# Kernel tuning notes

Measured on AMD Instinct MI355X. Metric: run time of the kernel, lower is better.

The kernel has to match this reference:

```python
import jax, jax.numpy as jnp
import numpy as np

N = 50000          # num nodes
E_RAND = 600000    # random edges (self-loops appended -> E = E_RAND + N)
HEADS = 4
OUT_CH = 16
OUT_NEURONS = 2 * OUT_CH   # diag reparam: [mean | std-logit]
IN_CH = 128
NEG_SLOPE = 0.2


def setup_inputs() -> dict:
    key = jax.random.key(0)
    k1, k2, k3, k4, k5 = jax.random.split(key, 5)
    x = jax.random.normal(k1, (N, IN_CH), jnp.float32)
    src = jax.random.randint(k2, (E_RAND,), 0, N, jnp.int32)
    dst = jax.random.randint(k3, (E_RAND,), 0, N, jnp.int32)
    loops = jnp.arange(N, dtype=jnp.int32)
    edge_index = jnp.stack([jnp.concatenate([src, loops]),
                            jnp.concatenate([dst, loops])])  # [2, E]
    # glorot init for weight [IN_CH, HEADS*OUT_NEURONS]
    s_w = float(np.sqrt(6.0 / (IN_CH + HEADS * OUT_NEURONS)))
    weight = jax.random.uniform(k4, (IN_CH, HEADS * OUT_NEURONS), jnp.float32, -s_w, s_w)
    # glorot for att [1, HEADS, 2*OUT_NEURONS]
    s_a = float(np.sqrt(6.0 / (HEADS + 2 * OUT_NEURONS)))
    att = jax.random.uniform(k5, (1, HEADS, 2 * OUT_NEURONS), jnp.float32, -s_a, s_a)
    bias = jnp.zeros((HEADS * OUT_NEURONS,), jnp.float32)
    return {"x": x, "edge_index": edge_index, "weight": weight, "att": att, "bias": bias}


def reference(x, edge_index, weight, att, bias):
    src, dst = edge_index[0], edge_index[1]  # j -> i (PyG source_to_target)
    h = (x @ weight).reshape(N, HEADS, OUT_NEURONS)          # Theta x
    x_j = h[src]                                             # [E, H, On]
    x_i = h[dst]                                             # [E, H, On]
    # alpha = LeakyReLU(a^T [x_i || x_j])
    alpha = (x_i * att[:, :, :OUT_NEURONS]).sum(-1) + \
            (x_j * att[:, :, OUT_NEURONS:]).sum(-1)          # [E, H]
    alpha = jax.nn.leaky_relu(alpha, NEG_SLOPE)
    # segment softmax over neighborhoods of target node i
    m = jax.ops.segment_max(alpha, dst, num_segments=N)      # [N, H]
    e = jnp.exp(alpha - m[dst])
    denom = jax.ops.segment_sum(e, dst, num_segments=N)      # [N, H]
    alpha = e / (denom[dst] + 1e-16)                          # [E, H]
    # scatter-add aggregation of attention-weighted features
    agg = jax.ops.segment_sum(x_j * alpha[:, :, None], dst, num_segments=N)  # [N, H, On]
    out = agg.reshape(N, HEADS * OUT_NEURONS) + bias
    # VIB diag reparameterization + closed-form KL against N(0, I)
    o = out.reshape(N * HEADS, OUT_NEURONS)
    mean = o[:, :OUT_CH]
    std = jax.nn.softplus(o[:, OUT_CH:] - 5.0) + 1e-10
    kl = (-jnp.log(std) + 0.5 * (std * std + mean * mean) - 0.5).sum(-1)  # [N*H]
    ixz = kl.reshape(N, HEADS).mean(-1)                      # [N]
    # eval + val_use_mean=True: output is the mean part
    out_final = mean.reshape(N, HEADS * OUT_CH)
    structure_kl_loss = jnp.zeros((), jnp.float32)
    return out_final, ixz, structure_kl_loss, mean, std
```

## Files before the change

kernel.cpp:

```cpp
#include <hip/hip_runtime.h>
#include <stdint.h>

#define NN 50000
#define NB 196
#define NEG_SLOPE 0.2f
#define WTS 136

#define IXZ_OFF    (NN * 64)
#define SKL_OFF    (NN * 64 + NN)
#define MEAN_OFF   (NN * 64 + NN + 1)
#define STD_OFF    (MEAN_OFF + NN * 64)

typedef unsigned int u32;
typedef unsigned short u16;
typedef __attribute__((ext_vector_type(8))) short short8;
typedef __attribute__((ext_vector_type(4))) float f32x4;

__device__ __forceinline__ float bf2f(u16 s) { return __uint_as_float(((u32)s) << 16); }
__device__ __forceinline__ u16 f2bf(float f) {
    u32 u = __float_as_uint(f);
    u += 0x7FFFu + ((u >> 16) & 1u);
    return (u16)(u >> 16);
}
__device__ __forceinline__ float lo16(u32 u) { return __uint_as_float(u << 16); }
__device__ __forceinline__ float hi16(u32 u) { return __uint_as_float(u & 0xFFFF0000u); }
__device__ __forceinline__ float red32(float v) {
    v += __shfl_xor(v, 16); v += __shfl_xor(v, 8); v += __shfl_xor(v, 4);
    v += __shfl_xor(v, 2);  v += __shfl_xor(v, 1);
    return v;
}
__device__ __forceinline__ float softplusf(float x) {
    return fmaxf(x, 0.f) + log1pf(expf(-fabsf(x)));
}
__device__ __forceinline__ void stout(void* o, long long idx, float v, bool f32) {
    if (f32) ((float*)o)[idx] = v;
    else     ((u16*)o)[idx]   = f2bf(v);
}
__device__ __forceinline__ int wscan_incl(int v, int lane) {
#pragma unroll
    for (int off = 1; off < 64; off <<= 1) {
        int u = __shfl_up(v, off);
        if (lane >= off) v += u;
    }
    return v;
}

__global__ void k_detect(const u32* __restrict__ xw, int* __restrict__ flag)
{
    int t = threadIdx.x;
    u32 wrd = xw[t];
    u32 e = (wrd >> 7) & 0xFF;
    bool plaus = (e >= 0x60 && e <= 0x85);
    unsigned long long b = __ballot(plaus);
    if (t == 0) flag[0] = (__popcll(b) < 32) ? 1 : 0;
}

__global__ __launch_bounds__(256) void k_wt(const void* __restrict__ wv_,
                                            const int* __restrict__ flag,
                                            u16* __restrict__ wtg)
{
    const int t = threadIdx.x;
    const int k = blockIdx.x * 16 + (t >> 4);
    const int cq = t & 15;
    const bool f32 = flag[0] != 0;
    u16 v[8];
    if (f32) {
        const float* w = (const float*)wv_;
        float4 a = *(const float4*)(w + k * 128 + cq * 8);
        float4 b = *(const float4*)(w + k * 128 + cq * 8 + 4);
        v[0] = f2bf(a.x); v[1] = f2bf(a.y); v[2] = f2bf(a.z); v[3] = f2bf(a.w);
        v[4] = f2bf(b.x); v[5] = f2bf(b.y); v[6] = f2bf(b.z); v[7] = f2bf(b.w);
    } else {
        const u16* w = (const u16*)wv_;
        uint4 u = *(const uint4*)(w + k * 128 + cq * 8);
        v[0] = (u16)(u.x & 0xFFFF); v[1] = (u16)(u.x >> 16);
        v[2] = (u16)(u.y & 0xFFFF); v[3] = (u16)(u.y >> 16);
        v[4] = (u16)(u.z & 0xFFFF); v[5] = (u16)(u.z >> 16);
        v[6] = (u16)(u.w & 0xFFFF); v[7] = (u16)(u.w >> 16);
    }
#pragma unroll
    for (int j = 0; j < 8; j++)
        wtg[(cq * 8 + j) * WTS + k] = v[j];
}

__global__ __launch_bounds__(256) void k_gemm(
    const void* __restrict__ xv, const u16* __restrict__ wtg,
    const void* __restrict__ attv, const int* __restrict__ flag,
    u16* __restrict__ hb, float* __restrict__ ai, float* __restrict__ aj)
{
    __shared__ __align__(16) u16 ls[128 * WTS];
    const int tid = threadIdx.x;
    const bool f32 = flag[0] != 0;

    {
        uint4* d = (uint4*)ls;
        const uint4* s = (const uint4*)wtg;
        for (int i = tid; i < 128 * WTS / 8; i += 256) d[i] = s[i];
    }

    const int w = tid >> 6, L = tid & 63;
    const int q = L >> 4, c15 = L & 15;
    const int nb16 = blockIdx.x * 64 + w * 16;

    short8 afr[4];
    {
        int nrow = nb16 + c15; if (nrow > NN - 1) nrow = NN - 1;
        if (f32) {
            const float* xp = (const float*)xv + (size_t)nrow * 128 + q * 8;
#pragma unroll
            for (int ks = 0; ks < 4; ks++) {
                float4 a = *(const float4*)(xp + ks * 32);
                float4 b = *(const float4*)(xp + ks * 32 + 4);
                union { short8 s; u16 e[8]; } u;
                u.e[0] = f2bf(a.x); u.e[1] = f2bf(a.y); u.e[2] = f2bf(a.z); u.e[3] = f2bf(a.w);
                u.e[4] = f2bf(b.x); u.e[5] = f2bf(b.y); u.e[6] = f2bf(b.z); u.e[7] = f2bf(b.w);
                afr[ks] = u.s;
            }
        } else {
            const u16* xp = (const u16*)xv + (size_t)nrow * 128 + q * 8;
#pragma unroll
            for (int ks = 0; ks < 4; ks++)
                afr[ks] = *(const short8*)(xp + ks * 32);
        }
    }
    __syncthreads();

    f32x4 acc[8];
#pragma unroll
    for (int t = 0; t < 8; t++) {
        acc[t] = (f32x4){0.f, 0.f, 0.f, 0.f};
        const u16* bp = ls + (16 * t + c15) * WTS + q * 8;
#pragma unroll
        for (int ks = 0; ks < 4; ks++) {
            short8 bfr = *(const short8*)(bp + ks * 32);
            acc[t] = __builtin_amdgcn_mfma_f32_16x16x32_bf16(afr[ks], bfr, acc[t], 0, 0, 0);
        }
    }

    float ati[8], atj[8];
#pragma unroll
    for (int t = 0; t < 8; t++) {
        int p = (t >> 1) * 64 + (t & 1) * 16 + c15;
        if (f32) {
            ati[t] = ((const float*)attv)[p];
            atj[t] = ((const float*)attv)[p + 32];
        } else {
            ati[t] = bf2f(((const u16*)attv)[p]);
            atj[t] = bf2f(((const u16*)attv)[p + 32]);
        }
    }
#pragma unroll
    for (int r = 0; r < 4; r++) {
        int node = nb16 + q * 4 + r;
#pragma unroll
        for (int h = 0; h < 4; h++) {
            float pi = acc[2 * h][r] * ati[2 * h] + acc[2 * h + 1][r] * ati[2 * h + 1];
            float pj = acc[2 * h][r] * atj[2 * h] + acc[2 * h + 1][r] * atj[2 * h + 1];
            pi += __shfl_xor(pi, 1); pj += __shfl_xor(pj, 1);
            pi += __shfl_xor(pi, 2); pj += __shfl_xor(pj, 2);
            pi += __shfl_xor(pi, 4); pj += __shfl_xor(pj, 4);
            pi += __shfl_xor(pi, 8); pj += __shfl_xor(pj, 8);
            if (c15 == 0 && node < NN) { ai[node * 4 + h] = pi; aj[node * 4 + h] = pj; }
        }
    }

    __syncthreads();
    u16* myls = ls + w * 16 * WTS;
#pragma unroll
    for (int t = 0; t < 8; t++)
#pragma unroll
        for (int r = 0; r < 4; r++)
            myls[(q * 4 + r) * WTS + 16 * t + c15] = f2bf(acc[t][r]);
#pragma unroll
    for (int v = 0; v < 4; v++) {
        int idx = v * 64 + L;
        int nrow = idx >> 4, c8 = idx & 15;
        int node = nb16 + nrow;
        if (node < NN)
            *(uint4*)(hb + (size_t)node * 128 + c8 * 8) =
                *(const uint4*)(myls + nrow * WTS + c8 * 8);
    }
}

__global__ __launch_bounds__(256) void k_count(const int* __restrict__ dst,
                                               int* __restrict__ counts, int E)
{
    int e = blockIdx.x * 256 + threadIdx.x;
    if (e < E) atomicAdd(&counts[dst[e]], 1);
}

__global__ __launch_bounds__(256) void k_scan1(const int* __restrict__ counts,
                                               int* __restrict__ lexcl,
                                               int* __restrict__ blocksum)
{
    __shared__ int wsum[4];
    const int t = threadIdx.x, lane = t & 63, wv = t >> 6;
    const int i = blockIdx.x * 256 + t;
    int c = (i < NN) ? counts[i] : 0;
    int inc = wscan_incl(c, lane);
    if (lane == 63) wsum[wv] = inc;
    __syncthreads();
    int add = 0;
#pragma unroll
    for (int k = 0; k < 3; k++) if (k < wv) add += wsum[k];
    inc += add;
    if (i < NN) lexcl[i] = inc - c;
    if (t == 255) blocksum[blockIdx.x] = inc;
}

__global__ __launch_bounds__(256) void k_scan2(const int* __restrict__ blocksum,
                                               int* __restrict__ blockoff)
{
    __shared__ int wsum[4];
    const int t = threadIdx.x, lane = t & 63, wv = t >> 6;
    int c = (t < NB) ? blocksum[t] : 0;
    int inc = wscan_incl(c, lane);
    if (lane == 63) wsum[wv] = inc;
    __syncthreads();
    int add = 0;
#pragma unroll
    for (int k = 0; k < 3; k++) if (k < wv) add += wsum[k];
    inc += add;
    if (t < NB) blockoff[t] = inc - c;
}

__global__ __launch_bounds__(256) void k_fill(
    const int* __restrict__ src, const int* __restrict__ dst,
    const int* __restrict__ lexcl, const int* __restrict__ blockoff,
    int* __restrict__ cursor, int* __restrict__ perm_src, int E)
{
    int e = blockIdx.x * 256 + threadIdx.x;
    if (e >= E) return;
    int d = dst[e];
    int pos = blockoff[d >> 8] + lexcl[d] + atomicAdd(&cursor[d], 1);
    perm_src[pos] = src[e];
}

__global__ __launch_bounds__(256) void k_agg(
    const int* __restrict__ lexcl, const int* __restrict__ blockoff,
    const int* __restrict__ counts, const int* __restrict__ perm_src,
    const float* __restrict__ ai, const float* __restrict__ aj,
    const u16* __restrict__ hb, const void* __restrict__ biasv,
    const int* __restrict__ flag, void* __restrict__ outv)
{
    const int t = blockIdx.x * 256 + threadIdx.x;
    const int node = t >> 5;
    if (node >= NN) return;
    const bool f32 = flag[0] != 0;
    const int l = t & 31;
    const int head = l >> 3;
    const int c4 = (l & 7) << 2;

    const int rs = blockoff[node >> 8] + lexcl[node];
    const int re = rs + counts[node];
    const float ain = ai[node * 4 + head];

    float dsum = 0.f, ax = 0.f, ay = 0.f, az = 0.f, aw = 0.f;
    for (int i = rs; i < re; i++) {
        int s = perm_src[i];
        float a = aj[s * 4 + head] + ain;
        a = a > 0.f ? a : NEG_SLOPE * a;
        float ev = __expf(a);
        dsum += ev;
        uint2 hv = *(const uint2*)(hb + (size_t)s * 128 + l * 4);
        ax += ev * lo16(hv.x); ay += ev * hi16(hv.x);
        az += ev * lo16(hv.y); aw += ev * hi16(hv.y);
    }
    const float inv = 1.f / (dsum + 1e-16f);
    const int cb = head * 32 + c4;
    float b0, b1, b2, b3;
    if (f32) {
        const float* bias = (const float*)biasv;
        b0 = bias[cb]; b1 = bias[cb + 1]; b2 = bias[cb + 2]; b3 = bias[cb + 3];
    } else {
        const u16* bias = (const u16*)biasv;
        b0 = bf2f(bias[cb]); b1 = bf2f(bias[cb + 1]);
        b2 = bf2f(bias[cb + 2]); b3 = bf2f(bias[cb + 3]);
    }
    float vx = ax * inv + b0;
    float vy = ay * inv + b1;
    float vz = az * inv + b2;
    float vw = aw * inv + b3;

    float part;
    if (c4 < 16) {
        part = 0.5f * (vx * vx + vy * vy + vz * vz + vw * vw);
        long long o = (long long)node * 64 + head * 16 + c4;
        stout(outv, o + 0, vx, f32); stout(outv, o + 1, vy, f32);
        stout(outv, o + 2, vz, f32); stout(outv, o + 3, vw, f32);
        long long om = (long long)MEAN_OFF + o;
        stout(outv, om + 0, vx, f32); stout(outv, om + 1, vy, f32);
        stout(outv, om + 2, vz, f32); stout(outv, om + 3, vw, f32);
    } else {
        float s0 = softplusf(vx - 5.f) + 1e-10f;
        float s1 = softplusf(vy - 5.f) + 1e-10f;
        float s2 = softplusf(vz - 5.f) + 1e-10f;
        float s3 = softplusf(vw - 5.f) + 1e-10f;
        part = (-logf(s0) + 0.5f * s0 * s0 - 0.5f)
             + (-logf(s1) + 0.5f * s1 * s1 - 0.5f)
             + (-logf(s2) + 0.5f * s2 * s2 - 0.5f)
             + (-logf(s3) + 0.5f * s3 * s3 - 0.5f);
        long long os = (long long)STD_OFF + (long long)node * 64 + head * 16 + (c4 - 16);
        stout(outv, os + 0, s0, f32); stout(outv, os + 1, s1, f32);
        stout(outv, os + 2, s2, f32); stout(outv, os + 3, s3, f32);
    }
    part = red32(part);
    if (l == 0) stout(outv, (long long)IXZ_OFF + node, part * 0.25f, f32);
    if (t == 0) stout(outv, (long long)SKL_OFF, 0.f, f32);
}

extern "C" void kernel_launch(void* const* d_in, const int* in_sizes, int n_in,
                              void* d_out, int out_size, void* d_ws, size_t ws_size,
                              hipStream_t stream)
{
    const void* x    = d_in[0];
    const int*  ei   = (const int*)d_in[1];
    const void* w    = d_in[2];
    const void* att  = d_in[3];
    const void* bias = d_in[4];

    const int E = in_sizes[1] / 2;
    const int* src = ei;
    const int* dst = ei + E;

    u16*   hb        = (u16*)d_ws;
    float* ai        = (float*)(hb + (size_t)NN * 128);
    float* aj        = ai + NN * 4;
    int*   perm_src  = (int*)(aj + NN * 4);
    int*   counts    = perm_src + E;
    int*   cursor    = counts + NN;
    int*   lexcl     = cursor + NN;
    int*   blocksum  = lexcl + NN;
    int*   blockoff  = blocksum + NB;
    int*   flag      = blockoff + NB;
    u16*   wtg       = (u16*)(flag + 1);

    k_detect<<<1, 64, 0, stream>>>((const u32*)x, flag);
    k_wt<<<8, 256, 0, stream>>>(w, flag, wtg);
    hipMemsetAsync(counts, 0, sizeof(int) * 2 * NN, stream);
    k_gemm<<<(NN + 63) / 64, 256, 0, stream>>>(x, wtg, att, flag, hb, ai, aj);
    k_count<<<(E + 255) / 256, 256, 0, stream>>>(dst, counts, E);
    k_scan1<<<NB, 256, 0, stream>>>(counts, lexcl, blocksum);
    k_scan2<<<1, 256, 0, stream>>>(blocksum, blockoff);
    k_fill<<<(E + 255) / 256, 256, 0, stream>>>(src, dst, lexcl, blockoff,
                                                cursor, perm_src, E);
    k_agg<<<(NN * 32 + 255) / 256, 256, 0, stream>>>(lexcl, blockoff, counts,
                                                     perm_src, ai, aj, hb, bias,
                                                     flag, d_out);
}
```

Baseline: 227.3 us.

## Fuse detect/memset into k_wt, count into gemm, widen agg to 16 lanes/node

Folds the dtype-detect kernel and the counts/cursor memset into k_wt, and moves the edge-count atomics into the tail of the GEMM kernel with a grid-stride loop. This removes three launches from the serial chain. The aggregation kernel now uses 16 lanes per node, each loading 8 bf16 channels with a uint4 and processing two edges per iteration. That gives more memory-level parallelism and halves the thread count, at the cost of more registers per thread.

```diff
diff --git a/kernel.cpp b/kernel.cpp
--- a/kernel.cpp
+++ b/kernel.cpp
@@ -24,11 +24,6 @@
 }
 __device__ __forceinline__ float lo16(u32 u) { return __uint_as_float(u << 16); }
 __device__ __forceinline__ float hi16(u32 u) { return __uint_as_float(u & 0xFFFF0000u); }
-__device__ __forceinline__ float red32(float v) {
-    v += __shfl_xor(v, 16); v += __shfl_xor(v, 8); v += __shfl_xor(v, 4);
-    v += __shfl_xor(v, 2);  v += __shfl_xor(v, 1);
-    return v;
-}
 __device__ __forceinline__ float softplusf(float x) {
     return fmaxf(x, 0.f) + log1pf(expf(-fabsf(x)));
 }
@@ -45,24 +40,33 @@
     return v;
 }
 
-__global__ void k_detect(const u32* __restrict__ xw, int* __restrict__ flag)
-{
-    int t = threadIdx.x;
-    u32 wrd = xw[t];
-    u32 e = (wrd >> 7) & 0xFF;
-    bool plaus = (e >= 0x60 && e <= 0x85);
-    unsigned long long b = __ballot(plaus);
-    if (t == 0) flag[0] = (__popcll(b) < 32) ? 1 : 0;
-}
-
-__global__ __launch_bounds__(256) void k_wt(const void* __restrict__ wv_,
-                                            const int* __restrict__ flag,
-                                            u16* __restrict__ wtg)
-{
+__global__ __launch_bounds__(256) void k_wt(const u32* __restrict__ xw,
+                                            const void* __restrict__ wv_,
+                                            int* __restrict__ flag,
+                                            u16* __restrict__ wtg,
+                                            int* __restrict__ zbase)
+{
+    __shared__ int lflag;
     const int t = threadIdx.x;
+    if (t < 64) {
+        u32 wrd = xw[t];
+        u32 e = (wrd >> 7) & 0xFF;
+        bool plaus = (e >= 0x60 && e <= 0x85);
+        unsigned long long b = __ballot(plaus);
+        if (t == 0) {
+            int f = (__popcll(b) < 32) ? 1 : 0;
+            lflag = f;
+            if (blockIdx.x == 0) flag[0] = f;
+        }
+    }
+    __syncthreads();
+    const bool f32 = lflag != 0;
+
+    const int gid = blockIdx.x * 256 + t;
+    for (int i = gid; i < 2 * NN; i += 8 * 256) zbase[i] = 0;
+
     const int k = blockIdx.x * 16 + (t >> 4);
     const int cq = t & 15;
-    const bool f32 = flag[0] != 0;
     u16 v[8];
     if (f32) {
         const float* w = (const float*)wv_;
@@ -86,7 +90,8 @@
 __global__ __launch_bounds__(256) void k_gemm(
     const void* __restrict__ xv, const u16* __restrict__ wtg,
     const void* __restrict__ attv, const int* __restrict__ flag,
-    u16* __restrict__ hb, float* __restrict__ ai, float* __restrict__ aj)
+    u16* __restrict__ hb, float* __restrict__ ai, float* __restrict__ aj,
+    const int* __restrict__ dst, int* __restrict__ counts, int E)
 {
     __shared__ __align__(16) u16 ls[128 * WTS];
     const int tid = threadIdx.x;
@@ -180,13 +185,11 @@
             *(uint4*)(hb + (size_t)node * 128 + c8 * 8) =
                 *(const uint4*)(myls + nrow * WTS + c8 * 8);
     }
-}
-
-__global__ __launch_bounds__(256) void k_count(const int* __restrict__ dst,
-                                               int* __restrict__ counts, int E)
-{
-    int e = blockIdx.x * 256 + threadIdx.x;
-    if (e < E) atomicAdd(&counts[dst[e]], 1);
+
+    const int gid = blockIdx.x * 256 + tid;
+    const int stride = gridDim.x * 256;
+    for (int e = gid; e < E; e += stride)
+        atomicAdd(&counts[dst[e]], 1);
 }
 
 __global__ __launch_bounds__(256) void k_scan1(const int* __restrict__ counts,
@@ -244,67 +247,91 @@
     const int* __restrict__ flag, void* __restrict__ outv)
 {
     const int t = blockIdx.x * 256 + threadIdx.x;
-    const int node = t >> 5;
+    const int node = t >> 4;
     if (node >= NN) return;
     const bool f32 = flag[0] != 0;
-    const int l = t & 31;
-    const int head = l >> 3;
-    const int c4 = (l & 7) << 2;
+    const int l = t & 15;
+    const int head = l >> 2;
+    const int cc0 = (l & 3) << 3;
 
     const int rs = blockoff[node >> 8] + lexcl[node];
     const int re = rs + counts[node];
     const float ain = ai[node * 4 + head];
-
-    float dsum = 0.f, ax = 0.f, ay = 0.f, az = 0.f, aw = 0.f;
-    for (int i = rs; i < re; i++) {
-        int s = perm_src[i];
-        float a = aj[s * 4 + head] + ain;
-        a = a > 0.f ? a : NEG_SLOPE * a;
-        float ev = __expf(a);
-        dsum += ev;
-        uint2 hv = *(const uint2*)(hb + (size_t)s * 128 + l * 4);
-        ax += ev * lo16(hv.x); ay += ev * hi16(hv.x);
-        az += ev * lo16(hv.y); aw += ev * hi16(hv.y);
-    }
+    const u16* hl8 = hb + l * 8;
+
+    float dsum = 0.f;
+    float a0 = 0.f, a1 = 0.f, a2 = 0.f, a3 = 0.f;
+    float a4 = 0.f, a5 = 0.f, a6 = 0.f, a7 = 0.f;
+
+    int i = rs;
+    for (; i + 1 < re; i += 2) {
+        int s0 = perm_src[i], s1 = perm_src[i + 1];
+        float x0 = aj[s0 * 4 + head] + ain;
+        float x1 = aj[s1 * 4 + head] + ain;
+        x0 = x0 > 0.f ? x0 : NEG_SLOPE * x0;
+        x1 = x1 > 0.f ? x1 : NEG_SLOPE * x1;
+        float e0 = __expf(x0), e1 = __expf(x1);
+        uint4 h0 = *(const uint4*)(hl8 + (size_t)s0 * 128);
+        uint4 h1 = *(const uint4*)(hl8 + (size_t)s1 * 128);
+        dsum += e0 + e1;
+        a0 += e0 * lo16(h0.x) + e1 * lo16(h1.x);
+        a1 += e0 * hi16(h0.x) + e1 * hi16(h1.x);
+        a2 += e0 * lo16(h0.y) + e1 * lo16(h1.y);
+        a3 += e0 * hi16(h0.y) + e1 * hi16(h1.y);
+        a4 += e0 * lo16(h0.z) + e1 * lo16(h1.z);
+        a5 += e0 * hi16(h0.z) + e1 * hi16(h1.z);
+        a6 += e0 * lo16(h0.w) + e1 * lo16(h1.w);
+        a7 += e0 * hi16(h0.w) + e1 * hi16(h1.w);
+    }
+    if (i < re) {
+        int s0 = perm_src[i];
+        float x0 = aj[s0 * 4 + head] + ain;
+        x0 = x0 > 0.f ? x0 : NEG_SLOPE * x0;
+        float e0 = __expf(x0);
+        uint4 h0 = *(const uint4*)(hl8 + (size_t)s0 * 128);
+        dsum += e0;
+        a0 += e0 * lo16(h0.x); a1 += e0 * hi16(h0.x);
+        a2 += e0 * lo16(h0.y); a3 += e0 * hi16(h0.y);
+        a4 += e0 * lo16(h0.z); a5 += e0 * hi16(h0.z);
+        a6 += e0 * lo16(h0.w); a7 += e0 * hi16(h0.w);
+    }
+
     const float inv = 1.f / (dsum + 1e-16f);
-    const int cb = head * 32 + c4;
-    float b0, b1, b2, b3;
+    const int cb = head * 32 + cc0;
+    float v[8];
     if (f32) {
         const float* bias = (const float*)biasv;
-        b0 = bias[cb]; b1 = bias[cb + 1]; b2 = bias[cb + 2]; b3 = bias[cb + 3];
+#pragma unroll
+        for (int j = 0; j < 8; j++) v[j] = bias[cb + j];
     } else {
         const u16* bias = (const u16*)biasv;
-        b0 = bf2f(bias[cb]); b1 = bf2f(bias[cb + 1]);
-        b2 = bf2f(bias[cb + 2]); b3 = bf2f(bias[cb + 3]);
-    }
-    float vx = ax * inv + b0;
-    float vy = ay * inv + b1;
-    float vz = az * inv + b2;
-    float vw = aw * inv + b3;
-
-    float part;
-    if (c4 < 16) {
-        part = 0.5f * (vx * vx + vy * vy + vz * vz + vw * vw);
-        long long o = (long long)node * 64 + head * 16 + c4;
-        stout(outv, o + 0, vx, f32); stout(outv, o + 1, vy, f32);
-        stout(outv, o + 2, vz, f32); stout(outv, o + 3, vw, f32);
+#pragma unroll
+        for (int j = 0; j < 8; j++) v[j] = bf2f(bias[cb + j]);
+    }
+    v[0] += a0 * inv; v[1] += a1 * inv; v[2] += a2 * inv; v[3] += a3 * inv;
+    v[4] += a4 * inv; v[5] += a5 * inv; v[6] += a6 * inv; v[7] += a7 * inv;
+
+    float part = 0.f;
+    if (cc0 < 16) {
+#pragma unroll
+        for (int j = 0; j < 8; j++) part += 0.5f * v[j] * v[j];
+        long long o = (long long)node * 64 + head * 16 + cc0;
+#pragma unroll
+        for (int j = 0; j < 8; j++) stout(outv, o + j, v[j], f32);
         long long om = (long long)MEAN_OFF + o;
-        stout(outv, om + 0, vx, f32); stout(outv, om + 1, vy, f32);
-        stout(outv, om + 2, vz, f32); stout(outv, om + 3, vw, f32);
+#pragma unroll
+        for (int j = 0; j < 8; j++) stout(outv, om + j, v[j], f32);
     } else {
-        float s0 = softplusf(vx - 5.f) + 1e-10f;
-        float s1 = softplusf(vy - 5.f) + 1e-10f;
-        float s2 = softplusf(vz - 5.f) + 1e-10f;
-        float s3 = softplusf(vw - 5.f) + 1e-10f;
-        part = (-logf(s0) + 0.5f * s0 * s0 - 0.5f)
-             + (-logf(s1) + 0.5f * s1 * s1 - 0.5f)
-             + (-logf(s2) + 0.5f * s2 * s2 - 0.5f)
-             + (-logf(s3) + 0.5f * s3 * s3 - 0.5f);
-        long long os = (long long)STD_OFF + (long long)node * 64 + head * 16 + (c4 - 16);
-        stout(outv, os + 0, s0, f32); stout(outv, os + 1, s1, f32);
-        stout(outv, os + 2, s2, f32); stout(outv, os + 3, s3, f32);
-    }
-    part = red32(part);
+        long long os = (long long)STD_OFF + (long long)node * 64 + head * 16 + (cc0 - 16);
+#pragma unroll
+        for (int j = 0; j < 8; j++) {
+            float s = softplusf(v[j] - 5.f) + 1e-10f;
+            part += -logf(s) + 0.5f * s * s - 0.5f;
+            stout(outv, os + j, s, f32);
+        }
+    }
+    part += __shfl_xor(part, 1); part += __shfl_xor(part, 2);
+    part += __shfl_xor(part, 4); part += __shfl_xor(part, 8);
     if (l == 0) stout(outv, (long long)IXZ_OFF + node, part * 0.25f, f32);
     if (t == 0) stout(outv, (long long)SKL_OFF, 0.f, f32);
 }
@@ -335,16 +362,14 @@
     int*   flag      = blockoff + NB;
     u16*   wtg       = (u16*)(flag + 1);
 
-    k_detect<<<1, 64, 0, stream>>>((const u32*)x, flag);
-    k_wt<<<8, 256, 0, stream>>>(w, flag, wtg);
-    hipMemsetAsync(counts, 0, sizeof(int) * 2 * NN, stream);
-    k_gemm<<<(NN + 63) / 64, 256, 0, stream>>>(x, wtg, att, flag, hb, ai, aj);
-    k_count<<<(E + 255) / 256, 256, 0, stream>>>(dst, counts, E);
+    k_wt<<<8, 256, 0, stream>>>((const u32*)x, w, flag, wtg, counts);
+    k_gemm<<<(NN + 63) / 64, 256, 0, stream>>>(x, wtg, att, flag, hb, ai, aj,
+                                               dst, counts, E);
     k_scan1<<<NB, 256, 0, stream>>>(counts, lexcl, blocksum);
     k_scan2<<<1, 256, 0, stream>>>(blocksum, blockoff);
     k_fill<<<(E + 255) / 256, 256, 0, stream>>>(src, dst, lexcl, blockoff,
                                                 cursor, perm_src, E);
-    k_agg<<<(NN * 32 + 255) / 256, 256, 0, stream>>>(lexcl, blockoff, counts,
+    k_agg<<<(NN * 16 + 255) / 256, 256, 0, stream>>>(lexcl, blockoff, counts,
                                                      perm_src, ai, aj, hb, bias,
                                                      flag, d_out);
 }
```

After: 210.0 us. -7.6%, faster.
